# Kernel tuning notes

Measured on AMD Instinct MI355X. Metric: run time of the kernel, lower is better.

Reference implementation:

```python
import jax, jax.numpy as jnp
import numpy as np

B, S, G, C = 4, 512, 48, 12
D = G * C            # d_model = 576, divisible by nhead=3
N = B * S * G        # 98304 graph nodes
E = N * 16           # 1572864 edges
H, FF = 3, 2048
HD = D // H
SCALE = 1.0 / float(np.sqrt(HD))


def _leaky(x):
    return jnp.where(x > 0, x, 0.2 * x)


def _ln(x, g, b):
    m = jnp.mean(x, -1, keepdims=True)
    v = jnp.var(x, -1, keepdims=True)
    return (x - m) * jax.lax.rsqrt(v + 1e-5) * g + b


def _conv(x, w, b, stride=1):
    # x: [B, Cin, L], w: [Cout, Cin, K]
    y = jax.lax.conv_general_dilated(x, w, (stride,), 'SAME',
                                     dimension_numbers=('NCH', 'OIH', 'NCH'))
    return y + b[None, :, None]


def _gat(x, src, dst, W, a_s, a_d, bias):
    # single-head GATConv (PyG defaults: self-loops already in src/dst, leaky 0.2)
    xp = x @ W.T                                            # [N, C]
    e = _leaky((xp @ a_s)[src] + (xp @ a_d)[dst])           # [E+N]
    m = jax.ops.segment_max(e, dst, num_segments=N)
    w = jnp.exp(e - m[dst])
    denom = jax.ops.segment_sum(w, dst, num_segments=N)
    alpha = w / denom[dst]
    return jax.ops.segment_sum(alpha[:, None] * xp[src], dst, num_segments=N) + bias


def _forward(edge_index, x, mask, noise,
             W_enc, a_src_enc, a_dst_enc, b_enc,
             Wq, bq, Wk, bk, Wv, bv, Wo, bo,
             ln1_g, ln1_b, W1, b1, W2, b2, ln2_g, ln2_b,
             enc1_w, enc1_b, down_w, down_b, bott_w, bott_b,
             up_w, up_b, dec_w, dec_b,
             W_dec, a_src_dec, a_dst_dec, b_dec):
    loops = jnp.arange(N)
    src = jnp.concatenate([edge_index[0], loops])
    dst = jnp.concatenate([edge_index[1], loops])
    # masked blend of observed data and imputation noise
    h = x * mask + noise * (1.0 - mask)
    h = _gat(h, src, dst, W_enc, a_src_enc, a_dst_enc, b_enc)       # [N, C]
    t = h.reshape(B, S, D)
    # TransformerEncoderLayer (post-norm, relu FFN, 3 heads)
    q = (t @ Wq.T + bq).reshape(B, S, H, HD)
    k = (t @ Wk.T + bk).reshape(B, S, H, HD)
    v = (t @ Wv.T + bv).reshape(B, S, H, HD)
    att = jax.nn.softmax(jnp.einsum('bqhd,bkhd->bhqk', q, k) * SCALE, axis=-1)
    o = jnp.einsum('bhqk,bkhd->bqhd', att, v).reshape(B, S, D) @ Wo.T + bo
    t = _ln(t + o, ln1_g, ln1_b)
    ff = jax.nn.relu(t @ W1.T + b1) @ W2.T + b2
    t = _ln(t + ff, ln2_g, ln2_b)
    # Unet1d auto-encoder over the time axis, channels = D
    y = t.transpose(0, 2, 1)                                        # [B, D, S]
    e1 = jax.nn.relu(_conv(y, enc1_w, enc1_b))                      # [B, D, S]
    d1 = jax.nn.relu(_conv(e1, down_w, down_b, 2))                  # [B, 2D, S/2]
    bt = jax.nn.relu(_conv(d1, bott_w, bott_b))                     # [B, 2D, S/2]
    up = jax.nn.relu(_conv(jnp.repeat(bt, 2, axis=2), up_w, up_b))  # [B, D, S]
    y = _conv(jnp.concatenate([up, e1], axis=1), dec_w, dec_b)      # [B, D, S]
    # GAT decoder + tanh
    h = y.transpose(0, 2, 1).reshape(N, C)
    h = _gat(h, src, dst, W_dec, a_src_dec, a_dst_dec, b_dec)
    return jnp.tanh(h)


def setup_inputs() -> dict:
    ks = iter(jax.random.split(jax.random.key(0), 64))
    def nrm(shape, s=0.2):
        return jax.random.normal(next(ks), shape, jnp.float32) * s
    return dict(
        edge_index=jax.random.randint(next(ks), (2, E), 0, N),
        x=jax.random.normal(next(ks), (N, C), jnp.float32),
        mask=(jax.random.uniform(next(ks), (N, C)) < 0.8).astype(jnp.float32),
        noise=jax.random.normal(next(ks), (N, C), jnp.float32),
        W_enc=nrm((C, C)), a_src_enc=nrm((C,)), a_dst_enc=nrm((C,)), b_enc=jnp.zeros((C,), jnp.float32),
        Wq=nrm((D, D), 0.05), bq=jnp.zeros((D,)), Wk=nrm((D, D), 0.05), bk=jnp.zeros((D,)),
        Wv=nrm((D, D), 0.05), bv=jnp.zeros((D,)), Wo=nrm((D, D), 0.05), bo=jnp.zeros((D,)),
        ln1_g=jnp.ones((D,)), ln1_b=jnp.zeros((D,)),
        W1=nrm((FF, D), 0.05), b1=jnp.zeros((FF,)), W2=nrm((D, FF), 0.05), b2=jnp.zeros((D,)),
        ln2_g=jnp.ones((D,)), ln2_b=jnp.zeros((D,)),
        enc1_w=nrm((D, D, 3), 0.03), enc1_b=jnp.zeros((D,)),
        down_w=nrm((2 * D, D, 3), 0.03), down_b=jnp.zeros((2 * D,)),
        bott_w=nrm((2 * D, 2 * D, 3), 0.02), bott_b=jnp.zeros((2 * D,)),
        up_w=nrm((D, 2 * D, 3), 0.02), up_b=jnp.zeros((D,)),
        dec_w=nrm((D, 2 * D, 3), 0.02), dec_b=jnp.zeros((D,)),
        W_dec=nrm((C, C)), a_src_dec=nrm((C,)), a_dst_dec=nrm((C,)), b_dec=jnp.zeros((C,), jnp.float32),
    )


def reference(edge_index, x, mask, noise,
              W_enc, a_src_enc, a_dst_enc, b_enc,
              Wq, bq, Wk, bk, Wv, bv, Wo, bo,
              ln1_g, ln1_b, W1, b1, W2, b2, ln2_g, ln2_b,
              enc1_w, enc1_b, down_w, down_b, bott_w, bott_b,
              up_w, up_b, dec_w, dec_b,
              W_dec, a_src_dec, a_dst_dec, b_dec):
    return _forward(edge_index, x, mask, noise,
                    W_enc, a_src_enc, a_dst_enc, b_enc,
                    Wq, bq, Wk, bk, Wv, bv, Wo, bo,
                    ln1_g, ln1_b, W1, b1, W2, b2, ln2_g, ln2_b,
                    enc1_w, enc1_b, down_w, down_b, bott_w, bott_b,
                    up_w, up_b, dec_w, dec_b,
                    W_dec, a_src_dec, a_dst_dec, b_dec)
```

## Files before the change

### kernel.cpp

```cpp
#include <hip/hip_runtime.h>
#include <hip/hip_bf16.h>
#include <math.h>

#define NN 98304
#define CC 12
#define EE 1572864
#define ETOT (EE + NN)
#define BB 4
#define SS 512
#define DD 576
#define HH 3
#define HDI 192
#define FFD 2048
#define MR (BB*SS)
#define ND (NN*CC)
#define ATT_SCALE 0.07216878364870323f
#define NB 768
#define BCAP 2560
#define BINBLK 192
#define BINCHUNK 8704

typedef __hip_bfloat16 bf;
typedef __attribute__((ext_vector_type(8))) short s8v;
typedef __attribute__((ext_vector_type(4))) short s4v;
typedef __attribute__((ext_vector_type(4))) float f4v;

__device__ __forceinline__ void gl16(const void* g, void* l) {
    __builtin_amdgcn_global_load_lds(
        (const __attribute__((address_space(1))) unsigned int*)g,
        (__attribute__((address_space(3))) unsigned int*)l, 16, 0, 0);
}
__device__ __forceinline__ short bfbits(float f) {
    bf t = __float2bfloat16(f);
    return *(short*)&t;
}
__device__ __forceinline__ unsigned pk2(float a, float b) {
    return (unsigned)(unsigned short)bfbits(a) |
           ((unsigned)(unsigned short)bfbits(b) << 16);
}
__device__ __forceinline__ float lo16(unsigned v) { return __uint_as_float(v << 16); }
__device__ __forceinline__ float hi16(unsigned v) { return __uint_as_float(v & 0xffff0000u); }

__global__ __launch_bounds__(256) void gat_node_k(
    const float* __restrict__ xin, const float* __restrict__ mask,
    const float* __restrict__ noise,
    const float* __restrict__ W, const float* __restrict__ a_s,
    const float* __restrict__ a_d,
    float4* __restrict__ rows, float* __restrict__ dval,
    int blend)
{
    int n = blockIdx.x * 256 + threadIdx.x;
    if (n >= NN) return;
    const float4* xr = (const float4*)(xin + (size_t)n*CC);
    float h[CC];
    float4 h0 = xr[0], h1 = xr[1], h2 = xr[2];
    h[0]=h0.x; h[1]=h0.y; h[2]=h0.z; h[3]=h0.w;
    h[4]=h1.x; h[5]=h1.y; h[6]=h1.z; h[7]=h1.w;
    h[8]=h2.x; h[9]=h2.y; h[10]=h2.z; h[11]=h2.w;
    if (blend) {
        const float4* mr = (const float4*)(mask  + (size_t)n*CC);
        const float4* nr = (const float4*)(noise + (size_t)n*CC);
        float m[CC], z[CC];
        float4 m0=mr[0],m1=mr[1],m2=mr[2], z0=nr[0],z1=nr[1],z2=nr[2];
        m[0]=m0.x;m[1]=m0.y;m[2]=m0.z;m[3]=m0.w;m[4]=m1.x;m[5]=m1.y;m[6]=m1.z;m[7]=m1.w;
        m[8]=m2.x;m[9]=m2.y;m[10]=m2.z;m[11]=m2.w;
        z[0]=z0.x;z[1]=z0.y;z[2]=z0.z;z[3]=z0.w;z[4]=z1.x;z[5]=z1.y;z[6]=z1.z;z[7]=z1.w;
        z[8]=z2.x;z[9]=z2.y;z[10]=z2.z;z[11]=z2.w;
#pragma unroll
        for (int c = 0; c < CC; ++c) h[c] = h[c]*m[c] + z[c]*(1.0f-m[c]);
    }
    float sv = 0.f, dv = 0.f;
    float o[CC];
#pragma unroll
    for (int oc = 0; oc < CC; ++oc) {
        float a = 0.f;
#pragma unroll
        for (int ic = 0; ic < CC; ++ic) a += h[ic]*W[oc*CC+ic];
        o[oc] = a;
        sv += a * a_s[oc]; dv += a * a_d[oc];
    }
    float4 r0, r1;
    r0.x = sv;
    r0.y = __uint_as_float(pk2(o[0], o[1]));
    r0.z = __uint_as_float(pk2(o[2], o[3]));
    r0.w = __uint_as_float(pk2(o[4], o[5]));
    r1.x = __uint_as_float(pk2(o[6], o[7]));
    r1.y = __uint_as_float(pk2(o[8], o[9]));
    r1.z = __uint_as_float(pk2(o[10], o[11]));
    r1.w = 0.f;
    rows[(size_t)n*2]   = r0;
    rows[(size_t)n*2+1] = r1;
    dval[n] = dv;
}

__global__ __launch_bounds__(256) void binA_k(
    const int* __restrict__ e0, const int* __restrict__ e1,
    int* __restrict__ bcnt, unsigned* __restrict__ pairs)
{
    __shared__ int lh[NB];
    __shared__ int lbase[NB];
    const int tid = threadIdx.x;
    const int lo = blockIdx.x * BINCHUNK;
    const int hi = lo + BINCHUNK;
#pragma unroll
    for (int b = tid; b < NB; b += 256) lh[b] = 0;
    __syncthreads();
    for (int i = lo + tid; i < hi; i += 256) {
        int d = (i < EE) ? e1[i] : (i - EE);
        atomicAdd(&lh[d >> 7], 1);
    }
    __syncthreads();
    for (int b = tid; b < NB; b += 256) {
        int c = lh[b];
        lbase[b] = c ? atomicAdd(&bcnt[b], c) : 0;
        lh[b] = 0;
    }
    __syncthreads();
    for (int i = lo + tid; i < hi; i += 256) {
        int s, d;
        if (i < EE) { s = e0[i]; d = e1[i]; }
        else        { s = i - EE; d = s; }
        int b = d >> 7;
        int p = lbase[b] + atomicAdd(&lh[b], 1);
        if (p < BCAP)
            pairs[(size_t)b*BCAP + p] = ((unsigned)(d & 127) << 17) | (unsigned)s;
    }
}

__global__ __launch_bounds__(1024) void binB_k(
    unsigned* __restrict__ pairs, const int* __restrict__ bcnt,
    int* __restrict__ cnt, int* __restrict__ offs)
{
    __shared__ unsigned ent[BCAP];
    __shared__ int lh[128], ls[128], lc[128];
    const int b = blockIdx.x, tid = threadIdx.x;
    const int n = min(bcnt[b], BCAP);
    for (int i = tid; i < n; i += 1024) ent[i] = pairs[(size_t)b*BCAP + i];
    if (tid < 128) lh[tid] = 0;
    __syncthreads();
    for (int i = tid; i < n; i += 1024) atomicAdd(&lh[ent[i] >> 17], 1);
    __syncthreads();
    if (tid == 0) { int run = 0; for (int j = 0; j < 128; ++j) { ls[j] = run; run += lh[j]; } }
    __syncthreads();
    if (tid < 128) {
        int node = b*128 + tid;
        cnt[node]  = lh[tid];
        offs[node] = b*BCAP + ls[tid];
        lc[tid]    = ls[tid];
    }
    __syncthreads();
    for (int i = tid; i < n; i += 1024) {
        unsigned v = ent[i];
        int dl = (int)(v >> 17);
        int p = atomicAdd(&lc[dl], 1);
        pairs[(size_t)b*BCAP + p] = v & 0x1FFFFu;
    }
}

__global__ __launch_bounds__(256) void gat_agg8_k(
    const unsigned* __restrict__ pairs, const int* __restrict__ cnt,
    const int* __restrict__ offs,
    const float4* __restrict__ rows, const float* __restrict__ dval,
    const float* __restrict__ bias,
    float* __restrict__ out, bf* __restrict__ outb, int dotanh)
{
    int g = blockIdx.x*32 + (threadIdx.x >> 3);
    int l = threadIdx.x & 7;
    if (g >= NN) return;
    int beg = offs[g], m = cnt[g];
    float dv = dval[g];
    float acc[CC] = {};
    float den = 0.f;
    for (int i = l; i < m; i += 8) {
        unsigned s = pairs[beg + i];
        float4 r0 = rows[(size_t)s*2];
        float4 r1 = rows[(size_t)s*2+1];
        float e = r0.x + dv;
        e = e > 0.f ? e : 0.2f*e;
        float w = __expf(e);
        den += w;
        unsigned p01 = __float_as_uint(r0.y), p23 = __float_as_uint(r0.z);
        unsigned p45 = __float_as_uint(r0.w), p67 = __float_as_uint(r1.x);
        unsigned p89 = __float_as_uint(r1.y), pab = __float_as_uint(r1.z);
        acc[0]  += w*lo16(p01); acc[1]  += w*hi16(p01);
        acc[2]  += w*lo16(p23); acc[3]  += w*hi16(p23);
        acc[4]  += w*lo16(p45); acc[5]  += w*hi16(p45);
        acc[6]  += w*lo16(p67); acc[7]  += w*hi16(p67);
        acc[8]  += w*lo16(p89); acc[9]  += w*hi16(p89);
        acc[10] += w*lo16(pab); acc[11] += w*hi16(pab);
    }
#pragma unroll
    for (int off = 1; off < 8; off <<= 1) {
        den += __shfl_xor(den, off);
#pragma unroll
        for (int c = 0; c < CC; ++c) acc[c] += __shfl_xor(acc[c], off);
    }
    if (l == 0) {
        float inv = 1.f / den;
        float r[CC];
#pragma unroll
        for (int c = 0; c < CC; ++c) {
            r[c] = acc[c]*inv + bias[c];
            if (dotanh) r[c] = tanhf(r[c]);
        }
        if (out) {
            float4* orow = (float4*)(out + (size_t)g*CC);
            orow[0] = make_float4(r[0],r[1],r[2],r[3]);
            orow[1] = make_float4(r[4],r[5],r[6],r[7]);
            orow[2] = make_float4(r[8],r[9],r[10],r[11]);
        }
        if (outb) {
            s4v* brow = (s4v*)(outb + (size_t)g*CC);
            s4v b0, b1, b2;
            b0[0]=bfbits(r[0]); b0[1]=bfbits(r[1]); b0[2]=bfbits(r[2]); b0[3]=bfbits(r[3]);
            b1[0]=bfbits(r[4]); b1[1]=bfbits(r[5]); b1[2]=bfbits(r[6]); b1[3]=bfbits(r[7]);
            b2[0]=bfbits(r[8]); b2[1]=bfbits(r[9]); b2[2]=bfbits(r[10]); b2[3]=bfbits(r[11]);
            brow[0]=b0; brow[1]=b1; brow[2]=b2;
        }
    }
}

template<int TBM>
__global__ __launch_bounds__(256) void gemm_bt(
    const bf* __restrict__ A, const bf* __restrict__ B,
    const float* __restrict__ bias, float* __restrict__ Cf, bf* __restrict__ Cb,
    int K, int lda, int ldb, int ldc,
    long long sA1, long long sA2, long long sB1, long long sB2,
    long long sC1, long long sC2, int bdiv, long long sBias,
    float scale, int relu)
{
    constexpr int MI = TBM/32;
    __shared__ bf As[TBM*32];
    __shared__ bf Bs[64*32];
    const int tid = threadIdx.x, lane = tid & 63, wave = tid >> 6;
    const int z = blockIdx.z, z1 = z / bdiv, z2 = z % bdiv;
    const bf* Ab = A + z1*sA1 + z2*sA2;
    const bf* Bb = B + z1*sB1 + z2*sB2;
    const int bm = blockIdx.y * TBM, bn = blockIdx.x * 64;
    const int l4 = lane >> 2;
    const int swz0 = (l4 >> 1) & 3;
    const int lc = (((lane & 3) ^ swz0) * 8);
    const int arow0 = wave*(TBM/4) + l4;
    const int brow  = wave*16 + l4;
    const int wm = wave >> 1, wn = wave & 1;
    const int fr = lane & 15;
    const int gsw = (((lane >> 4) ^ ((fr >> 1) & 3)) * 8);
    f4v acc[MI][2] = {};

    for (int k0 = 0; k0 < K; k0 += 32) {
        gl16(Ab + (size_t)(bm + arow0)*lda + k0 + lc, As + wave*(TBM/4)*32);
        if constexpr (TBM == 128)
            gl16(Ab + (size_t)(bm + arow0 + 16)*lda + k0 + lc, As + wave*1024 + 512);
        gl16(Bb + (size_t)(bn + brow )*ldb + k0 + lc, Bs + wave*512);
        __syncthreads();
        s8v af[MI], bfv[2];
#pragma unroll
        for (int mi = 0; mi < MI; ++mi)
            af[mi] = *(const s8v*)&As[(wm*(TBM/2) + mi*16 + fr)*32 + gsw];
#pragma unroll
        for (int nj = 0; nj < 2; ++nj)
            bfv[nj] = *(const s8v*)&Bs[(wn*32 + nj*16 + fr)*32 + gsw];
#pragma unroll
        for (int mi = 0; mi < MI; ++mi)
#pragma unroll
            for (int nj = 0; nj < 2; ++nj)
                acc[mi][nj] = __builtin_amdgcn_mfma_f32_16x16x32_bf16(
                    af[mi], bfv[nj], acc[mi][nj], 0, 0, 0);
        __syncthreads();
    }

    float* Cfb = Cf ? Cf + z1*sC1 + z2*sC2 : nullptr;
    bf*    Cbb = Cb ? Cb + z1*sC1 + z2*sC2 : nullptr;
    const float* bp = bias ? bias + z1*sBias : nullptr;
#pragma unroll
    for (int mi = 0; mi < MI; ++mi) {
#pragma unroll
        for (int nj = 0; nj < 2; ++nj) {
            int col = bn + wn*32 + nj*16 + fr;
            float bv = bp ? bp[col] : 0.f;
#pragma unroll
            for (int r = 0; r < 4; ++r) {
                int row = bm + wm*(TBM/2) + mi*16 + (lane>>4)*4 + r;
                float vv = (acc[mi][nj][r] + bv) * scale;
                if (relu) vv = fmaxf(vv, 0.f);
                if (Cfb) Cfb[(size_t)row*ldc + col] = vv;
                if (Cbb) Cbb[(size_t)row*ldc + col] = __float2bfloat16(vv);
            }
        }
    }
}

template<int CIN, int MODE>
__global__ __launch_bounds__(256) void conv_bt(
    const bf* __restrict__ A0, const bf* __restrict__ A1,
    const bf* __restrict__ Bw, float* __restrict__ Cpart,
    int K, int M, int N, int Lout, int Lin, int splitk)
{
    __shared__ bf As[64*32];
    __shared__ bf Bs[64*32];
    const int tid = threadIdx.x, lane = tid & 63, wave = tid >> 6;
    const int bm = blockIdx.y * 64, bn = blockIdx.x * 64;
    const int kchunk = K / splitk;
    const int kbeg = blockIdx.z * kchunk, kend = kbeg + kchunk;
    const int l4 = lane >> 2;
    const int swz0 = (l4 >> 1) & 3;
    const int lc = (((lane & 3) ^ swz0) * 8);
    const int arow = bm + wave*16 + l4;
    const int brow = bn + wave*16 + l4;
    const int ab = arow / Lout, al = arow % Lout;
    const int wm = wave >> 1, wn = wave & 1;
    const int fr = lane & 15;
    const int gsw = (((lane >> 4) ^ ((fr >> 1) & 3)) * 8);
    f4v acc[2][2] = {};

    for (int k0 = kbeg; k0 < kend; k0 += 32) {
        int kk  = k0 / CIN;
        int ci0 = k0 - kk*CIN;
        int row;
        if constexpr (MODE == 1)      row = 2*al + kk + 1;
        else if constexpr (MODE == 2) row = (al + kk + 1) >> 1;
        else                          row = al + kk;
        const bf* src;
        if constexpr (MODE == 3) {
            constexpr int CH = CIN/2;
            bool lohalf = ci0 < CH;
            src = (lohalf ? A0 : A1)
                + ((size_t)(ab*(Lin+2) + row))*CH + (lohalf ? ci0 : ci0 - CH);
        } else {
            src = A0 + ((size_t)(ab*(Lin+2) + row))*CIN + ci0;
        }
        gl16(src + lc, As + wave*512);
        gl16(Bw + (size_t)brow*K + k0 + lc, Bs + wave*512);
        __syncthreads();
        s8v af[2], bfv[2];
#pragma unroll
        for (int mi = 0; mi < 2; ++mi)
            af[mi] = *(const s8v*)&As[(wm*32 + mi*16 + fr)*32 + gsw];
#pragma unroll
        for (int nj = 0; nj < 2; ++nj)
            bfv[nj] = *(const s8v*)&Bs[(wn*32 + nj*16 + fr)*32 + gsw];
#pragma unroll
        for (int mi = 0; mi < 2; ++mi)
#pragma unroll
            for (int nj = 0; nj < 2; ++nj)
                acc[mi][nj] = __builtin_amdgcn_mfma_f32_16x16x32_bf16(
                    af[mi], bfv[nj], acc[mi][nj], 0, 0, 0);
        __syncthreads();
    }

    float* Cp = Cpart + (size_t)blockIdx.z * M * N;
#pragma unroll
    for (int mi = 0; mi < 2; ++mi)
#pragma unroll
        for (int nj = 0; nj < 2; ++nj) {
            int col = bn + wn*32 + nj*16 + fr;
#pragma unroll
            for (int r = 0; r < 4; ++r) {
                int row = bm + wm*32 + mi*16 + (lane>>4)*4 + r;
                Cp[(size_t)row*N + col] = acc[mi][nj][r];
            }
        }
}

__global__ __launch_bounds__(256) void convepi_k(
    const float* __restrict__ part, const float* __restrict__ bias,
    bf* __restrict__ outb, float* __restrict__ outf,
    int M, int N, int Lout, int relu)
{
    int total = M * (N >> 3);
    int i = blockIdx.x*256 + threadIdx.x;
    if (i >= total) return;
    int c8 = (i % (N >> 3)) * 8;
    int row = i / (N >> 3);
    const float* p0 = part + (size_t)row*N + c8;
    const float* p1 = p0 + (size_t)M*N;
    float v[8];
#pragma unroll
    for (int j = 0; j < 8; ++j) {
        float t = p0[j] + p1[j] + bias[c8+j];
        v[j] = relu ? fmaxf(t, 0.f) : t;
    }
    if (outb) {
        int b = row / Lout, l = row % Lout;
        s8v pk;
#pragma unroll
        for (int j = 0; j < 8; ++j) pk[j] = bfbits(v[j]);
        *(s8v*)&outb[((size_t)(b*(Lout+2) + l + 1))*N + c8] = pk;
    }
    if (outf) {
        float4* o = (float4*)(outf + (size_t)row*N + c8);
        o[0] = make_float4(v[0],v[1],v[2],v[3]);
        o[1] = make_float4(v[4],v[5],v[6],v[7]);
    }
}

struct PZJob { bf* p; int Lin; int Cin; };
struct PZJobs { PZJob j[5]; };
__global__ __launch_bounds__(256) void padzero_k(PZJobs J)
{
    PZJob jb = J.j[blockIdx.y];
    int n8 = BB * 2 * (jb.Cin >> 3);
    for (int i = blockIdx.x*256 + threadIdx.x; i < n8; i += gridDim.x*256) {
        int c8 = i % (jb.Cin >> 3); int r = i / (jb.Cin >> 3);
        int b = r >> 1; int row = (r & 1) ? (jb.Lin + 1) : 0;
        s8v z = {0,0,0,0,0,0,0,0};
        *(s8v*)&jb.p[((size_t)(b*(jb.Lin+2) + row))*jb.Cin + c8*8] = z;
    }
}

__global__ __launch_bounds__(256) void softmax_k(
    const float* __restrict__ S, bf* __restrict__ P)
{
    int row = blockIdx.x; size_t base = (size_t)row * SS;
    int tid = threadIdx.x;
    __shared__ float red[256];
    float v0 = S[base+tid], v1 = S[base+tid+256];
    red[tid] = fmaxf(v0, v1); __syncthreads();
    for (int off = 128; off > 0; off >>= 1) {
        if (tid < off) red[tid] = fmaxf(red[tid], red[tid+off]);
        __syncthreads();
    }
    float mx = red[0]; __syncthreads();
    float e0 = __expf(v0-mx), e1 = __expf(v1-mx);
    red[tid] = e0+e1; __syncthreads();
    for (int off = 128; off > 0; off >>= 1) {
        if (tid < off) red[tid] += red[tid+off];
        __syncthreads();
    }
    float inv = 1.f / red[0];
    P[base+tid]     = __float2bfloat16(e0*inv);
    P[base+tid+256] = __float2bfloat16(e1*inv);
}

__global__ __launch_bounds__(256) void vtrans_k(
    const bf* __restrict__ vb, bf* __restrict__ vt)
{
    int idx = blockIdx.x*256 + threadIdx.x;
    int z = idx / (HDI*(SS/8)); int r = idx % (HDI*(SS/8));
    int d = r / (SS/8); int s8 = (r % (SS/8))*8;
    int b = z / HH, h = z % HH;
    s8v ov;
#pragma unroll
    for (int j = 0; j < 8; ++j) {
        bf t = vb[((size_t)(b*SS + s8 + j))*DD + h*HDI + d];
        ov[j] = *(short*)&t;
    }
    *(s8v*)&vt[(size_t)z*HDI*SS + (size_t)d*SS + s8] = ov;
}

struct CJob { const float* src; unsigned short* dst; float* dstf; int n4; };
struct CJobs { CJob j[9]; };
__global__ __launch_bounds__(256) void castmany_k(CJobs J)
{
    CJob jb = J.j[blockIdx.y];
    for (int i = blockIdx.x*256 + threadIdx.x; i < jb.n4; i += gridDim.x*256) {
        float4 v = ((const float4*)jb.src)[i];
        if (jb.dst) {
            s4v p;
            p[0]=bfbits(v.x); p[1]=bfbits(v.y); p[2]=bfbits(v.z); p[3]=bfbits(v.w);
            ((s4v*)jb.dst)[i] = p;
        } else {
            ((float4*)jb.dstf)[i] = v;
        }
    }
}

__global__ __launch_bounds__(256) void ln_k(
    const float* __restrict__ a, const float* __restrict__ r,
    const float* __restrict__ g, const float* __restrict__ be,
    float* __restrict__ out, bf* __restrict__ ob, int padout)
{
    int row = blockIdx.x; int tid = threadIdx.x;
    __shared__ float red[256], red2[256];
    size_t base = (size_t)row * DD;
    size_t base2 = padout ? ((size_t)(row + 2*(row/SS) + 1))*DD : base;
    float x0 = a[base+tid]      + r[base+tid];
    float x1 = a[base+tid+256]  + r[base+tid+256];
    float x2 = (tid < 64) ? (a[base+tid+512] + r[base+tid+512]) : 0.f;
    float s  = x0+x1+x2;
    float s2 = x0*x0 + x1*x1 + x2*x2;
    red[tid] = s; red2[tid] = s2; __syncthreads();
    for (int off = 128; off > 0; off >>= 1) {
        if (tid < off) { red[tid] += red[tid+off]; red2[tid] += red2[tid+off]; }
        __syncthreads();
    }
    float mean = red[0] / (float)DD;
    float var  = red2[0] / (float)DD - mean*mean;
    float inv = rsqrtf(var + 1e-5f);
    float y0 = (x0-mean)*inv*g[tid]     + be[tid];
    float y1 = (x1-mean)*inv*g[tid+256] + be[tid+256];
    if (out) { out[base+tid] = y0; out[base+tid+256] = y1; }
    if (ob)  { ob[base2+tid] = __float2bfloat16(y0); ob[base2+tid+256] = __float2bfloat16(y1); }
    if (tid < 64) {
        float y2 = (x2-mean)*inv*g[tid+512] + be[tid+512];
        if (out) out[base+tid+512] = y2;
        if (ob)  ob[base2+tid+512] = __float2bfloat16(y2);
    }
}

__global__ __launch_bounds__(256) void wtrans_k(
    const float* __restrict__ w, bf* __restrict__ wT, int Cout, int Cin)
{
    int n8 = Cout * 3 * (Cin >> 3);
    for (int i = blockIdx.x*256 + threadIdx.x; i < n8; i += gridDim.x*256) {
        int c8 = i % (Cin >> 3); int r = i / (Cin >> 3);
        int kk = r % 3; int co = r / 3;
        int ci = c8 * 8;
        s8v ov;
#pragma unroll
        for (int j = 0; j < 8; ++j)
            ov[j] = bfbits(w[((size_t)co*Cin + ci + j)*3 + kk]);
        *(s8v*)&wT[(size_t)co*3*Cin + (size_t)kk*Cin + ci] = ov;
    }
}

extern "C" void kernel_launch(void* const* d_in, const int* in_sizes, int n_in,
                              void* d_out, int out_size, void* d_ws, size_t ws_size,
                              hipStream_t stream)
{
    const int*   edge   = (const int*)  d_in[0];
    const float* x      = (const float*)d_in[1];
    const float* mask   = (const float*)d_in[2];
    const float* noise  = (const float*)d_in[3];
    const float* W_enc  = (const float*)d_in[4];
    const float* asrc_e = (const float*)d_in[5];
    const float* adst_e = (const float*)d_in[6];
    const float* b_enc  = (const float*)d_in[7];
    const float* Wq = (const float*)d_in[8];  const float* bq = (const float*)d_in[9];
    const float* Wk = (const float*)d_in[10]; const float* bk = (const float*)d_in[11];
    const float* Wv = (const float*)d_in[12]; const float* bv = (const float*)d_in[13];
    const float* Wo = (const float*)d_in[14]; const float* bo = (const float*)d_in[15];
    const float* ln1g = (const float*)d_in[16]; const float* ln1b = (const float*)d_in[17];
    const float* W1 = (const float*)d_in[18]; const float* b1 = (const float*)d_in[19];
    const float* W2 = (const float*)d_in[20]; const float* b2 = (const float*)d_in[21];
    const float* ln2g = (const float*)d_in[22]; const float* ln2b = (const float*)d_in[23];
    const float* enc1_w = (const float*)d_in[24]; const float* enc1_b = (const float*)d_in[25];
    const float* down_w = (const float*)d_in[26]; const float* down_b = (const float*)d_in[27];
    const float* bott_w = (const float*)d_in[28]; const float* bott_b = (const float*)d_in[29];
    const float* up_w   = (const float*)d_in[30]; const float* up_b   = (const float*)d_in[31];
    const float* dec_w  = (const float*)d_in[32]; const float* dec_b  = (const float*)d_in[33];
    const float* W_dec  = (const float*)d_in[34];
    const float* asrc_d = (const float*)d_in[35];
    const float* adst_d = (const float*)d_in[36];
    const float* b_dec  = (const float*)d_in[37];
    float* out = (float*)d_out;

    float* ws = (float*)d_ws;
    float4*   rows  = (float4*)ws;
    float*    dval  = ws + 786432;
    int*      cnt   = (int*)(ws + 884736);
    int*      offs  = (int*)(ws + 983040);
    unsigned* pairs = (unsigned*)(ws + 1376256);
    int*      bcnt  = (int*)(ws + 3342336);
    float*    t     = ws + 3343360;
    bf*       tb    = (bf*)(ws + 4523008);
    bf*       qb    = (bf*)(ws + 5112832);
    bf*       kb    = (bf*)(ws + 5702656);
    bf*       vb    = (bf*)(ws + 6292480);
    float*    big   = ws + 6882304;
    float*    scores = big;
    bf*       Pb    = (bf*)(big + 3145728);
    bf*       wTbott = (bf*)big;
    float*    parts  = big + 1990656;
    float*    o     = ws + 11600896;
    float*    t1    = ws + 12780544;
    bf*       t1b   = (bf*)(ws + 13960192);
    bf*       ff1b  = (bf*)(ws + 14550016);
    bf*       t2p   = (bf*)(ws + 16647168);
    bf*       e1p   = (bf*)(ws + 17239296);
    bf*       d1p   = (bf*)(ws + 17831424);
    bf*       btbp  = (bf*)(ws + 18425856);
    bf*       upp   = (bf*)(ws + 19020288);
    float*    dec   = ws + 19612416;
    bf*       wTb   = (bf*)(ws + 20792064);
    bf*       Wqb   = (bf*)(ws + 21787392);
    bf*       Wkb   = (bf*)(ws + 21953280);
    bf*       Wvb   = (bf*)(ws + 22119168);
    bf*       Wob   = (bf*)(ws + 22285056);
    bf*       W1b   = (bf*)(ws + 22450944);
    bf*       W2b   = (bf*)(ws + 23040768);
    float*    biasQKV = ws + 23630592;
    bf*       vt    = kb;
    bf*       attnO = qb;

    const int* e0 = edge;
    const int* e1i = edge + EE;

    hipMemsetAsync(bcnt, 0, NB*sizeof(int), stream);
    binA_k<<<BINBLK, 256, 0, stream>>>(e0, e1i, bcnt, pairs);
    binB_k<<<NB, 1024, 0, stream>>>(pairs, bcnt, cnt, offs);

    {
        PZJobs Z;
        Z.j[0] = { t2p, 512, 576 };
        Z.j[1] = { e1p, 512, 576 };
        Z.j[2] = { d1p, 256, 1152 };
        Z.j[3] = { btbp, 256, 1152 };
        Z.j[4] = { upp, 512, 576 };
        padzero_k<<<dim3(5, 5), 256, 0, stream>>>(Z);
    }

    {
        CJobs J;
        J.j[0] = { Wq, (unsigned short*)Wqb, nullptr, DD*DD/4 };
        J.j[1] = { Wk, (unsigned short*)Wkb, nullptr, DD*DD/4 };
        J.j[2] = { Wv, (unsigned short*)Wvb, nullptr, DD*DD/4 };
        J.j[3] = { Wo, (unsigned short*)Wob, nullptr, DD*DD/4 };
        J.j[4] = { W1, (unsigned short*)W1b, nullptr, FFD*DD/4 };
        J.j[5] = { W2, (unsigned short*)W2b, nullptr, FFD*DD/4 };
        J.j[6] = { bq, nullptr, biasQKV,        DD/4 };
        J.j[7] = { bk, nullptr, biasQKV + DD,   DD/4 };
        J.j[8] = { bv, nullptr, biasQKV + 2*DD, DD/4 };
        castmany_k<<<dim3(576, 9), 256, 0, stream>>>(J);
    }

    gat_node_k<<<NN/256, 256, 0, stream>>>(x, mask, noise, W_enc, asrc_e, adst_e,
                                           rows, dval, 1);
    gat_agg8_k<<<NN/32, 256, 0, stream>>>(pairs, cnt, offs, rows, dval, b_enc,
                                          t, tb, 0);

    gemm_bt<128><<<dim3(9,16,3), 256, 0, stream>>>(tb, Wqb, biasQKV, nullptr, qb,
        DD, DD, DD, DD,
        0,0, (long long)DD*DD,0, (long long)MR*DD,0, 1, DD, 1.f, 0);
    gemm_bt<128><<<dim3(8,4,12), 256, 0, stream>>>(qb, kb, nullptr, scores, nullptr,
        HDI, DD, DD, SS,
        (long long)SS*DD, HDI, (long long)SS*DD, HDI,
        3LL*SS*SS, (long long)SS*SS, HH, 0, ATT_SCALE, 0);
    softmax_k<<<12*SS, 256, 0, stream>>>(scores, Pb);
    vtrans_k<<<12*HDI*(SS/8)/256, 256, 0, stream>>>(vb, vt);
    gemm_bt<64><<<dim3(3,8,12), 256, 0, stream>>>(Pb, vt, nullptr, nullptr, attnO,
        SS, SS, SS, DD,
        3LL*SS*SS, (long long)SS*SS, 3LL*HDI*SS, (long long)HDI*SS,
        (long long)SS*DD, HDI, HH, 0, 1.f, 0);
    gemm_bt<64><<<dim3(9,32,1), 256, 0, stream>>>(attnO, Wob, bo, o, nullptr,
        DD, DD, DD, DD, 0,0,0,0,0,0, 1, 0, 1.f, 0);
    ln_k<<<MR, 256, 0, stream>>>(t, o, ln1g, ln1b, t1, t1b, 0);
    gemm_bt<128><<<dim3(32,16,1), 256, 0, stream>>>(t1b, W1b, b1, nullptr, ff1b,
        DD, DD, DD, FFD, 0,0,0,0,0,0, 1, 0, 1.f, 1);
    gemm_bt<64><<<dim3(9,32,1), 256, 0, stream>>>(ff1b, W2b, b2, o, nullptr,
        FFD, FFD, FFD, DD, 0,0,0,0,0,0, 1, 0, 1.f, 0);
    ln_k<<<MR, 256, 0, stream>>>(t1, o, ln2g, ln2b, nullptr, t2p, 1);

    wtrans_k<<<(576*3*72+255)/256, 256, 0, stream>>>(enc1_w, wTb, 576, 576);
    conv_bt<576,0><<<dim3(9,32,2), 256, 0, stream>>>(t2p, nullptr, wTb, parts,
        1728, 2048, 576, 512, 512, 2);
    convepi_k<<<576, 256, 0, stream>>>(parts, enc1_b, e1p, nullptr, 2048, 576, 512, 1);
    wtrans_k<<<(1152*3*72+255)/256, 256, 0, stream>>>(down_w, wTb, 1152, 576);
    conv_bt<576,1><<<dim3(18,16,2), 256, 0, stream>>>(e1p, nullptr, wTb, parts,
        1728, 1024, 1152, 256, 512, 2);
    convepi_k<<<576, 256, 0, stream>>>(parts, down_b, d1p, nullptr, 1024, 1152, 256, 1);
    wtrans_k<<<(1152*3*144+255)/256, 256, 0, stream>>>(bott_w, wTbott, 1152, 1152);
    conv_bt<1152,0><<<dim3(18,16,2), 256, 0, stream>>>(d1p, nullptr, wTbott, parts,
        3456, 1024, 1152, 256, 256, 2);
    convepi_k<<<576, 256, 0, stream>>>(parts, bott_b, btbp, nullptr, 1024, 1152, 256, 1);
    wtrans_k<<<(576*3*144+255)/256, 256, 0, stream>>>(up_w, wTb, 576, 1152);
    conv_bt<1152,2><<<dim3(9,32,2), 256, 0, stream>>>(btbp, nullptr, wTb, parts,
        3456, 2048, 576, 512, 256, 2);
    convepi_k<<<576, 256, 0, stream>>>(parts, up_b, upp, nullptr, 2048, 576, 512, 1);
    wtrans_k<<<(576*3*144+255)/256, 256, 0, stream>>>(dec_w, wTb, 576, 1152);
    conv_bt<1152,3><<<dim3(9,32,2), 256, 0, stream>>>(upp, e1p, wTb, parts,
        3456, 2048, 576, 512, 512, 2);
    convepi_k<<<576, 256, 0, stream>>>(parts, dec_b, nullptr, dec, 2048, 576, 512, 0);

    gat_node_k<<<NN/256, 256, 0, stream>>>(dec, nullptr, nullptr, W_dec, asrc_d, adst_d,
                                           rows, dval, 0);
    gat_agg8_k<<<NN/32, 256, 0, stream>>>(pairs, cnt, offs, rows, dval, b_dec,
                                          out, nullptr, 1);
}
```

Baseline: 400.4 us.

## Split edge binning into count/scan/scatter and raise conv split-K factor

Edge binning now runs as three kernels: a per-block histogram, a per-bin prefix scan across 512 blocks, and a scatter using precomputed bases. This replaces the global atomic base allocation and the memset, and the larger block count gives more parallelism, but binning now makes two passes over the edge list. The conv GEMMs raise the split-K factor from 2 to 3 or 4 to fill more CUs. The epilogue is generalised to sum nsplit partials, which adds partial-buffer traffic, and the partials buffer moves to a region aliased with o.

Result: faster. 372.0 us (-7.1%).

```diff
diff --git a/kernel.cpp b/kernel.cpp
--- a/kernel.cpp
+++ b/kernel.cpp
@@ -17,8 +17,8 @@
 #define ATT_SCALE 0.07216878364870323f
 #define NB 768
 #define BCAP 2560
-#define BINBLK 192
-#define BINCHUNK 8704
+#define BINB2 512
+#define CHUNK2 3264
 
 typedef __hip_bfloat16 bf;
 typedef __attribute__((ext_vector_type(8))) short s8v;
@@ -93,16 +93,12 @@
     dval[n] = dv;
 }
 
-__global__ __launch_bounds__(256) void binA_k(
-    const int* __restrict__ e0, const int* __restrict__ e1,
-    int* __restrict__ bcnt, unsigned* __restrict__ pairs)
+__global__ __launch_bounds__(256) void binA1_k(
+    const int* __restrict__ e1, int* __restrict__ gcnt)
 {
     __shared__ int lh[NB];
-    __shared__ int lbase[NB];
     const int tid = threadIdx.x;
-    const int lo = blockIdx.x * BINCHUNK;
-    const int hi = lo + BINCHUNK;
-#pragma unroll
+    const int lo = blockIdx.x * CHUNK2, hi = lo + CHUNK2;
     for (int b = tid; b < NB; b += 256) lh[b] = 0;
     __syncthreads();
     for (int i = lo + tid; i < hi; i += 256) {
@@ -110,9 +106,37 @@
         atomicAdd(&lh[d >> 7], 1);
     }
     __syncthreads();
+    for (int b = tid; b < NB; b += 256)
+        gcnt[(size_t)blockIdx.x*NB + b] = lh[b];
+}
+
+__global__ __launch_bounds__(512) void binscan_k(
+    const int* __restrict__ gcnt, int* __restrict__ gbase, int* __restrict__ bcnt)
+{
+    __shared__ int sh[BINB2];
+    const int b = blockIdx.x, t = threadIdx.x;
+    int v = gcnt[(size_t)t*NB + b];
+    sh[t] = v; __syncthreads();
+    for (int off = 1; off < BINB2; off <<= 1) {
+        int add = (t >= off) ? sh[t-off] : 0;
+        __syncthreads();
+        sh[t] += add;
+        __syncthreads();
+    }
+    gbase[(size_t)b*BINB2 + t] = sh[t] - v;
+    if (t == BINB2-1) bcnt[b] = sh[BINB2-1];
+}
+
+__global__ __launch_bounds__(256) void binA2_k(
+    const int* __restrict__ e0, const int* __restrict__ e1,
+    const int* __restrict__ gbase, unsigned* __restrict__ pairs)
+{
+    __shared__ int lbase[NB];
+    __shared__ int lh[NB];
+    const int tid = threadIdx.x;
+    const int lo = blockIdx.x * CHUNK2, hi = lo + CHUNK2;
     for (int b = tid; b < NB; b += 256) {
-        int c = lh[b];
-        lbase[b] = c ? atomicAdd(&bcnt[b], c) : 0;
+        lbase[b] = gbase[(size_t)b*BINB2 + blockIdx.x];
         lh[b] = 0;
     }
     __syncthreads();
@@ -365,20 +389,24 @@
 __global__ __launch_bounds__(256) void convepi_k(
     const float* __restrict__ part, const float* __restrict__ bias,
     bf* __restrict__ outb, float* __restrict__ outf,
-    int M, int N, int Lout, int relu)
+    int M, int N, int Lout, int relu, int nsplit)
 {
     int total = M * (N >> 3);
     int i = blockIdx.x*256 + threadIdx.x;
     if (i >= total) return;
     int c8 = (i % (N >> 3)) * 8;
     int row = i / (N >> 3);
-    const float* p0 = part + (size_t)row*N + c8;
-    const float* p1 = p0 + (size_t)M*N;
     float v[8];
 #pragma unroll
-    for (int j = 0; j < 8; ++j) {
-        float t = p0[j] + p1[j] + bias[c8+j];
-        v[j] = relu ? fmaxf(t, 0.f) : t;
+    for (int j = 0; j < 8; ++j) v[j] = bias[c8+j];
+    for (int z = 0; z < nsplit; ++z) {
+        const float* p = part + (size_t)z*M*N + (size_t)row*N + c8;
+#pragma unroll
+        for (int j = 0; j < 8; ++j) v[j] += p[j];
+    }
+    if (relu) {
+#pragma unroll
+        for (int j = 0; j < 8; ++j) v[j] = fmaxf(v[j], 0.f);
     }
     if (outb) {
         int b = row / Lout, l = row % Lout;
@@ -558,11 +586,13 @@
     bf*       kb    = (bf*)(ws + 5702656);
     bf*       vb    = (bf*)(ws + 6292480);
     float*    big   = ws + 6882304;
+    int*      gcnt  = (int*)big;
+    int*      gbase = (int*)(big + 393216);
     float*    scores = big;
     bf*       Pb    = (bf*)(big + 3145728);
     bf*       wTbott = (bf*)big;
-    float*    parts  = big + 1990656;
     float*    o     = ws + 11600896;
+    float*    parts = ws + 11600896;
     float*    t1    = ws + 12780544;
     bf*       t1b   = (bf*)(ws + 13960192);
     bf*       ff1b  = (bf*)(ws + 14550016);
@@ -586,8 +616,9 @@
     const int* e0 = edge;
     const int* e1i = edge + EE;
 
-    hipMemsetAsync(bcnt, 0, NB*sizeof(int), stream);
-    binA_k<<<BINBLK, 256, 0, stream>>>(e0, e1i, bcnt, pairs);
+    binA1_k<<<BINB2, 256, 0, stream>>>(e1i, gcnt);
+    binscan_k<<<NB, BINB2, 0, stream>>>(gcnt, gbase, bcnt);
+    binA2_k<<<BINB2, 256, 0, stream>>>(e0, e1i, gbase, pairs);
     binB_k<<<NB, 1024, 0, stream>>>(pairs, bcnt, cnt, offs);
 
     {
@@ -642,25 +673,25 @@
     ln_k<<<MR, 256, 0, stream>>>(t1, o, ln2g, ln2b, nullptr, t2p, 1);
 
     wtrans_k<<<(576*3*72+255)/256, 256, 0, stream>>>(enc1_w, wTb, 576, 576);
-    conv_bt<576,0><<<dim3(9,32,2), 256, 0, stream>>>(t2p, nullptr, wTb, parts,
-        1728, 2048, 576, 512, 512, 2);
-    convepi_k<<<576, 256, 0, stream>>>(parts, enc1_b, e1p, nullptr, 2048, 576, 512, 1);
+    conv_bt<576,0><<<dim3(9,32,3), 256, 0, stream>>>(t2p, nullptr, wTb, parts,
+        1728, 2048, 576, 512, 512, 3);
+    convepi_k<<<576, 256, 0, stream>>>(parts, enc1_b, e1p, nullptr, 2048, 576, 512, 1, 3);
     wtrans_k<<<(1152*3*72+255)/256, 256, 0, stream>>>(down_w, wTb, 1152, 576);
-    conv_bt<576,1><<<dim3(18,16,2), 256, 0, stream>>>(e1p, nullptr, wTb, parts,
-        1728, 1024, 1152, 256, 512, 2);
-    convepi_k<<<576, 256, 0, stream>>>(parts, down_b, d1p, nullptr, 1024, 1152, 256, 1);
+    conv_bt<576,1><<<dim3(18,16,3), 256, 0, stream>>>(e1p, nullptr, wTb, parts,
+        1728, 1024, 1152, 256, 512, 3);
+    convepi_k<<<576, 256, 0, stream>>>(parts, down_b, d1p, nullptr, 1024, 1152, 256, 1, 3);
     wtrans_k<<<(1152*3*144+255)/256, 256, 0, stream>>>(bott_w, wTbott, 1152, 1152);
-    conv_bt<1152,0><<<dim3(18,16,2), 256, 0, stream>>>(d1p, nullptr, wTbott, parts,
-        3456, 1024, 1152, 256, 256, 2);
-    convepi_k<<<576, 256, 0, stream>>>(parts, bott_b, btbp, nullptr, 1024, 1152, 256, 1);
+    conv_bt<1152,0><<<dim3(18,16,4), 256, 0, stream>>>(d1p, nullptr, wTbott, parts,
+        3456, 1024, 1152, 256, 256, 4);
+    convepi_k<<<576, 256, 0, stream>>>(parts, bott_b, btbp, nullptr, 1024, 1152, 256, 1, 4);
     wtrans_k<<<(576*3*144+255)/256, 256, 0, stream>>>(up_w, wTb, 576, 1152);
-    conv_bt<1152,2><<<dim3(9,32,2), 256, 0, stream>>>(btbp, nullptr, wTb, parts,
-        3456, 2048, 576, 512, 256, 2);
-    convepi_k<<<576, 256, 0, stream>>>(parts, up_b, upp, nullptr, 2048, 576, 512, 1);
+    conv_bt<1152,2><<<dim3(9,32,4), 256, 0, stream>>>(btbp, nullptr, wTb, parts,
+        3456, 2048, 576, 512, 256, 4);
+    convepi_k<<<576, 256, 0, stream>>>(parts, up_b, upp, nullptr, 2048, 576, 512, 1, 4);
     wtrans_k<<<(576*3*144+255)/256, 256, 0, stream>>>(dec_w, wTb, 576, 1152);
-    conv_bt<1152,3><<<dim3(9,32,2), 256, 0, stream>>>(upp, e1p, wTb, parts,
-        3456, 2048, 576, 512, 512, 2);
-    convepi_k<<<576, 256, 0, stream>>>(parts, dec_b, nullptr, dec, 2048, 576, 512, 0);
+    conv_bt<1152,3><<<dim3(9,32,4), 256, 0, stream>>>(upp, e1p, wTb, parts,
+        3456, 2048, 576, 512, 512, 4);
+    convepi_k<<<576, 256, 0, stream>>>(parts, dec_b, nullptr, dec, 2048, 576, 512, 0, 4);
 
     gat_node_k<<<NN/256, 256, 0, stream>>>(dec, nullptr, nullptr, W_dec, asrc_d, adst_d,
                                            rows, dval, 0);
```
